# Optimization experiments

Measured on AMD Instinct MI355X. Metric: run time of the kernel, lower is better.

Reference implementation:

```python
import jax, jax.numpy as jnp
import numpy as np

N = 50000      # nodes
E = 800000     # edges (avg degree 16)
D_IN = 128
HID = [128, 64, 32]
C = 2
EPS = 1e-5


def _lin(k, fan_in, fan_out):
    return jax.random.normal(k, (fan_in, fan_out), jnp.float32) / np.float32(np.sqrt(fan_in))


def setup_inputs() -> dict:
    key = jax.random.key(0)
    ks = jax.random.split(key, 40)
    inp = {}
    inp["x"] = jax.random.normal(ks[0], (N, D_IN), jnp.float32)
    inp["edge_index"] = jax.random.randint(ks[1], (2, E), 0, N, dtype=jnp.int32)
    i = 2
    dims = [D_IN] + HID
    for l in range(3):
        di, do = dims[l], dims[l + 1]
        inp[f"W{l}"] = _lin(ks[i], di, do); i += 1
        inp[f"b{l}"] = jnp.zeros((do,), jnp.float32)
        inp[f"bn{l}_g"] = jnp.ones((do,), jnp.float32)
        inp[f"bn{l}_b"] = jnp.zeros((do,), jnp.float32)
        inp[f"bn{l}_m"] = 0.1 * jax.random.normal(ks[i], (do,), jnp.float32); i += 1
        inp[f"bn{l}_v"] = 0.5 + jax.random.uniform(ks[i], (do,), jnp.float32); i += 1
        if di != do:
            inp[f"skip{l}_W"] = _lin(ks[i], di, do); i += 1
            inp[f"skip{l}_b"] = jnp.zeros((do,), jnp.float32)
    inp["cls1_W"] = _lin(ks[i], HID[-1], HID[-1] // 2); i += 1
    inp["cls1_b"] = jnp.zeros((HID[-1] // 2,), jnp.float32)
    inp["cls2_W"] = _lin(ks[i], HID[-1] // 2, C); i += 1
    inp["cls2_b"] = jnp.zeros((C,), jnp.float32)
    return inp


def _gcn_conv(x, W, b, src, dst):
    # PyG GCNConv: add self loops, symmetric deg^{-1/2} normalization.
    h = x @ W                                            # [N, do]
    deg = jax.ops.segment_sum(jnp.ones((E,), h.dtype), dst, num_segments=N) + 1.0  # self loop
    dinv = jax.lax.rsqrt(deg)                            # deg >= 1
    norm = dinv[src] * dinv[dst]                         # [E]
    agg = jax.ops.segment_sum(h[src] * norm[:, None], dst, num_segments=N)
    return agg + h * (dinv * dinv)[:, None] + b          # self-loop msg + bias


def _bn(x, g, b, m, v):
    return (x - m) * jax.lax.rsqrt(v + EPS) * g + b


def reference(x, edge_index,
              W0, b0, bn0_g, bn0_b, bn0_m, bn0_v,
              W1, b1, bn1_g, bn1_b, bn1_m, bn1_v, skip1_W, skip1_b,
              W2, b2, bn2_g, bn2_b, bn2_m, bn2_v, skip2_W, skip2_b,
              cls1_W, cls1_b, cls2_W, cls2_b):
    src, dst = edge_index[0], edge_index[1]
    # layer 0: skip is Identity (128 -> 128)
    res = x
    h = jax.nn.relu(_bn(_gcn_conv(x, W0, b0, src, dst), bn0_g, bn0_b, bn0_m, bn0_v))
    h = h + res
    # layer 1: 128 -> 64, linear skip
    res = h @ skip1_W + skip1_b
    h = jax.nn.relu(_bn(_gcn_conv(h, W1, b1, src, dst), bn1_g, bn1_b, bn1_m, bn1_v))
    h = h + res
    # layer 2: 64 -> 32, linear skip
    res = h @ skip2_W + skip2_b
    h = jax.nn.relu(_bn(_gcn_conv(h, W2, b2, src, dst), bn2_g, bn2_b, bn2_m, bn2_v))
    h = h + res
    # classifier (dropout inactive at inference)
    h = jax.nn.relu(h @ cls1_W + cls1_b)
    logits = h @ cls2_W + cls2_b
    return jax.nn.log_softmax(logits, axis=1)
```

## Files before the change

### kernel.cpp

```cpp
#include <hip/hip_runtime.h>
#include <hip/hip_bf16.h>
#include <math.h>


#define BN_EPS 1e-5f

typedef __attribute__((ext_vector_type(8))) short bf16x8;
typedef __attribute__((ext_vector_type(4))) float f32x4;

static __device__ __forceinline__ float bf2f(unsigned int u16) {
    return __uint_as_float(u16 << 16);
}
static __device__ __forceinline__ unsigned short f2bf(float f) {
    unsigned int b = __float_as_uint(f);
    return (unsigned short)((b + 0x7FFFu + ((b >> 16) & 1u)) >> 16);
}
static __device__ __forceinline__ unsigned int pack2(float a, float b) {
    return (unsigned int)f2bf(a) | ((unsigned int)f2bf(b) << 16);
}
static __device__ __forceinline__ void unpack8(uint4 u, float* f) {
    f[0] = bf2f(u.x & 0xffffu); f[1] = bf2f(u.x >> 16);
    f[2] = bf2f(u.y & 0xffffu); f[3] = bf2f(u.y >> 16);
    f[4] = bf2f(u.z & 0xffffu); f[5] = bf2f(u.z >> 16);
    f[6] = bf2f(u.w & 0xffffu); f[7] = bf2f(u.w >> 16);
}
static __device__ __forceinline__ int swz(int row, int kb, int rowb) {
    return row * rowb + (kb ^ ((row & 7) << 4));
}

__global__ void prep_kernel(int* __restrict__ counts, int N, int nbZero,
                            const float* __restrict__ W0,
                            const float* __restrict__ W1, const float* __restrict__ sk1W,
                            const float* __restrict__ W2, const float* __restrict__ sk2W,
                            unsigned short* __restrict__ Wt0,
                            unsigned short* __restrict__ Wt1,
                            unsigned short* __restrict__ Wt2)
{
    int b = blockIdx.x, tid = threadIdx.x;
    if (b < nbZero) {
        int i = b * 256 + tid;
        if (i < N) counts[i] = 0;
        return;
    }
    b -= nbZero;
    if (b < 64) {
        int idx = b * 256 + tid;
        int m = idx >> 7, k = idx & 127;
        Wt0[idx] = f2bf(W0[(size_t)k * 128 + m]);
        return;
    }
    b -= 64;
    if (b < 64) {
        int idx = b * 256 + tid;
        int m = idx >> 7, k = idx & 127;
        float v = (m < 64) ? W1[(size_t)k * 64 + m] : sk1W[(size_t)k * 64 + (m - 64)];
        Wt1[idx] = f2bf(v);
        return;
    }
    b -= 64;
    {
        int idx = b * 256 + tid;
        int m = idx >> 6, k = idx & 63;
        float v = (m < 32) ? W2[(size_t)k * 32 + m] : sk2W[(size_t)k * 32 + (m - 32)];
        Wt2[idx] = f2bf(v);
    }
}

__global__ void rank_hist_kernel(const int* __restrict__ dst, int* __restrict__ counts,
                                 int* __restrict__ rank, int E) {
    int base = (blockIdx.x * 256 + threadIdx.x) * 4;
    if (base + 3 < E) {
        int4 d = *(const int4*)(dst + base);
        int4 r;
        r.x = atomicAdd(&counts[d.x], 1);
        r.y = atomicAdd(&counts[d.y], 1);
        r.z = atomicAdd(&counts[d.z], 1);
        r.w = atomicAdd(&counts[d.w], 1);
        *(int4*)(rank + base) = r;
    } else {
        for (int e = base; e < E; ++e) rank[e] = atomicAdd(&counts[dst[e]], 1);
    }
}

__global__ void scan_block_kernel(const int* __restrict__ counts, int* __restrict__ excl,
                                  int* __restrict__ bsum, int N) {
    __shared__ int s[256];
    int tid = threadIdx.x;
    int i = blockIdx.x * 256 + tid;
    int v = (i < N) ? counts[i] : 0;
    s[tid] = v;
    __syncthreads();
#pragma unroll
    for (int off = 1; off < 256; off <<= 1) {
        int t = (tid >= off) ? s[tid - off] : 0;
        __syncthreads();
        s[tid] += t;
        __syncthreads();
    }
    if (i < N) excl[i] = s[tid] - v;
    if (tid == 255) bsum[blockIdx.x] = s[255];
}

__global__ void scan_add_kernel(const int* __restrict__ excl, const int* __restrict__ bsum,
                                const int* __restrict__ counts,
                                int* __restrict__ rowptr, float* __restrict__ dinv,
                                int nb, int N, int E) {
    __shared__ int sb[256];
    int tid = threadIdx.x;
    int v = (tid < nb) ? bsum[tid] : 0;
    sb[tid] = v;
    __syncthreads();
#pragma unroll
    for (int off = 1; off < 256; off <<= 1) {
        int t = (tid >= off) ? sb[tid - off] : 0;
        __syncthreads();
        sb[tid] += t;
        __syncthreads();
    }
    int eb = sb[blockIdx.x] - ((blockIdx.x < nb) ? bsum[blockIdx.x] : 0);
    int i = blockIdx.x * 256 + tid;
    if (i < N) {
        rowptr[i] = excl[i] + eb;
        dinv[i]   = rsqrtf((float)counts[i] + 1.0f);
    }
    if (i == N) rowptr[N] = E;
}

__global__ void fill_csr_kernel(const int* __restrict__ src, const int* __restrict__ dst,
                                const int* __restrict__ rank, const int* __restrict__ rowptr,
                                int* __restrict__ csr, int E) {
    int base = (blockIdx.x * 256 + threadIdx.x) * 4;
    if (base + 3 < E) {
        int4 s = *(const int4*)(src + base);
        int4 d = *(const int4*)(dst + base);
        int4 r = *(const int4*)(rank + base);
        csr[rowptr[d.x] + r.x] = s.x;
        csr[rowptr[d.y] + r.y] = s.y;
        csr[rowptr[d.z] + r.z] = s.z;
        csr[rowptr[d.w] + r.w] = s.w;
    } else {
        for (int e = base; e < E; ++e) csr[rowptr[dst[e]] + rank[e]] = src[e];
    }
}

template <int K, int M1, int M2, bool IN_BF16>
__launch_bounds__(256)
__global__ void mfma_gemm_kernel(const float* __restrict__ Xf,
                                 const unsigned short* __restrict__ Xb,
                                 const unsigned short* __restrict__ Wt,
                                 const float* __restrict__ skb,
                                 unsigned short* __restrict__ H,
                                 unsigned short* __restrict__ SK, int N)
{
    constexpr int M    = M1 + M2;
    constexpr int BM   = 8192 / M;
    constexpr int WC   = M / 64;
    constexpr int ROWB = K * 2;
    constexpr int CPR  = K / 8;
    constexpr int WCH  = (M * K) / 2048;

    __shared__ unsigned char XsB[BM * K * 2];
    __shared__ unsigned char WsB[M * K * 2];

    const int tid = threadIdx.x;
    const int r0  = blockIdx.x * BM;

#pragma unroll
    for (int c = 0; c < 4; ++c) {
        int q   = tid + 256 * c;
        int row = q / CPR, kq = q % CPR;
        int grow = r0 + row;
        uint4 u = make_uint4(0u, 0u, 0u, 0u);
        if (IN_BF16) {
            if (grow < N) u = *(const uint4*)(Xb + (size_t)grow * K + kq * 8);
        } else {
            if (grow < N) {
                const float* p = Xf + (size_t)grow * K + kq * 8;
                float4 v0 = *(const float4*)p;
                float4 v1 = *(const float4*)(p + 4);
                u.x = pack2(v0.x, v0.y); u.y = pack2(v0.z, v0.w);
                u.z = pack2(v1.x, v1.y); u.w = pack2(v1.z, v1.w);
            }
        }
        *(uint4*)(XsB + swz(row, kq * 16, ROWB)) = u;
    }
#pragma unroll
    for (int c = 0; c < WCH; ++c) {
        int q = tid + 256 * c;
        int m = q / CPR, kq = q % CPR;
        uint4 u = *(const uint4*)(Wt + (size_t)m * K + kq * 8);
        *(uint4*)(WsB + swz(m, kq * 16, ROWB)) = u;
    }
    __syncthreads();

    const int lane = tid & 63, wid = tid >> 6;
    const int wr = wid / WC, wc = wid % WC;
    const int lrow = lane & 15;
    const int kb   = (lane >> 4) << 4;

    f32x4 acc[2][4];
#pragma unroll
    for (int fi = 0; fi < 2; ++fi)
#pragma unroll
        for (int fj = 0; fj < 4; ++fj)
            acc[fi][fj] = (f32x4){0.f, 0.f, 0.f, 0.f};

#pragma unroll
    for (int ks = 0; ks < K / 32; ++ks) {
        const int kb0 = ks * 64 + kb;
        bf16x8 a0 = *(const bf16x8*)(XsB + swz(wr * 32 +      lrow, kb0, ROWB));
        bf16x8 a1 = *(const bf16x8*)(XsB + swz(wr * 32 + 16 + lrow, kb0, ROWB));
        bf16x8 b0 = *(const bf16x8*)(WsB + swz(wc * 64 +      lrow, kb0, ROWB));
        bf16x8 b1 = *(const bf16x8*)(WsB + swz(wc * 64 + 16 + lrow, kb0, ROWB));
        bf16x8 b2 = *(const bf16x8*)(WsB + swz(wc * 64 + 32 + lrow, kb0, ROWB));
        bf16x8 b3 = *(const bf16x8*)(WsB + swz(wc * 64 + 48 + lrow, kb0, ROWB));
        acc[0][0] = __builtin_amdgcn_mfma_f32_16x16x32_bf16(a0, b0, acc[0][0], 0, 0, 0);
        acc[0][1] = __builtin_amdgcn_mfma_f32_16x16x32_bf16(a0, b1, acc[0][1], 0, 0, 0);
        acc[0][2] = __builtin_amdgcn_mfma_f32_16x16x32_bf16(a0, b2, acc[0][2], 0, 0, 0);
        acc[0][3] = __builtin_amdgcn_mfma_f32_16x16x32_bf16(a0, b3, acc[0][3], 0, 0, 0);
        acc[1][0] = __builtin_amdgcn_mfma_f32_16x16x32_bf16(a1, b0, acc[1][0], 0, 0, 0);
        acc[1][1] = __builtin_amdgcn_mfma_f32_16x16x32_bf16(a1, b1, acc[1][1], 0, 0, 0);
        acc[1][2] = __builtin_amdgcn_mfma_f32_16x16x32_bf16(a1, b2, acc[1][2], 0, 0, 0);
        acc[1][3] = __builtin_amdgcn_mfma_f32_16x16x32_bf16(a1, b3, acc[1][3], 0, 0, 0);
    }

    const int orow0 = r0 + wr * 32 + (lane >> 4) * 4;
#pragma unroll
    for (int fi = 0; fi < 2; ++fi) {
#pragma unroll
        for (int fj = 0; fj < 4; ++fj) {
            const int col = wc * 64 + fj * 16 + lrow;
            const bool conv = (M2 == 0) || (col < M1);
            const float sb = conv ? 0.f : skb[col - M1];
#pragma unroll
            for (int r = 0; r < 4; ++r) {
                const int row = orow0 + fi * 16 + r;
                if (row >= N) continue;
                const float val = acc[fi][fj][r];
                if (conv) H[(size_t)row * M1 + col] = f2bf(val);
                else      SK[(size_t)row * M2 + (col - M1)] = f2bf(val + sb);
            }
        }
    }
}

template <int M, bool OUT_BF16, bool RES_BF16, bool CLS>
__launch_bounds__(256)
__global__ void gather_bn_kernel(const int* __restrict__ rowptr, const int* __restrict__ csr,
                                 const unsigned short* __restrict__ H,
                                 const float* __restrict__ dinv,
                                 const float* __restrict__ bias,
                                 const float* __restrict__ g, const float* __restrict__ b,
                                 const float* __restrict__ m, const float* __restrict__ v,
                                 const void* __restrict__ res, void* __restrict__ out,
                                 const float* __restrict__ cW1, const float* __restrict__ cB1,
                                 const float* __restrict__ cW2, const float* __restrict__ cB2,
                                 int N)
{
    constexpr int TPN = M / 16;
    __shared__ float w1s[512];
    __shared__ float b1s[16];
    __shared__ float w2s[32];
    __shared__ float b2s[2];

    const int tid = threadIdx.x;
    if constexpr (CLS) {
        w1s[tid]       = cW1[tid];
        w1s[tid + 256] = cW1[tid + 256];
        if (tid < 16) b1s[tid] = cB1[tid];
        if (tid < 32) w2s[tid] = cW2[tid];
        if (tid < 2)  b2s[tid] = cB2[tid];
        __syncthreads();
    }

    int gid = blockIdx.x * 256 + tid;
    int n = gid / TPN;
    if (n >= N) return;
    const int c = (gid % TPN) * 16;

    float s[16], o[16];
#pragma unroll
    for (int q = 0; q < 4; ++q) {
        float4 gv = *(const float4*)&g[c + q * 4];
        float4 bv = *(const float4*)&b[c + q * 4];
        float4 mv = *(const float4*)&m[c + q * 4];
        float4 vv = *(const float4*)&v[c + q * 4];
        float4 iv = *(const float4*)&bias[c + q * 4];
        float sv[4] = {gv.x * rsqrtf(vv.x + BN_EPS), gv.y * rsqrtf(vv.y + BN_EPS),
                       gv.z * rsqrtf(vv.z + BN_EPS), gv.w * rsqrtf(vv.w + BN_EPS)};
        float bb[4] = {bv.x, bv.y, bv.z, bv.w};
        float mm[4] = {mv.x, mv.y, mv.z, mv.w};
        float ii[4] = {iv.x, iv.y, iv.z, iv.w};
#pragma unroll
        for (int q2 = 0; q2 < 4; ++q2) {
            s[q * 4 + q2] = sv[q2];
            o[q * 4 + q2] = (ii[q2] - mm[q2]) * sv[q2] + bb[q2];
        }
    }

    const float dn = dinv[n];
    float acc[16];
    {
        uint4 h0 = *(const uint4*)&H[(size_t)n * M + c];
        uint4 h1 = *(const uint4*)&H[(size_t)n * M + c + 8];
        float hf[16];
        unpack8(h0, hf); unpack8(h1, hf + 8);
        const float d2 = dn * dn;
#pragma unroll
        for (int k = 0; k < 16; ++k) acc[k] = hf[k] * d2;
    }

    int p   = rowptr[n];
    int end = rowptr[n + 1];
    for (; p + 3 < end; p += 4) {
        int s0 = csr[p], s1 = csr[p + 1], s2 = csr[p + 2], s3 = csr[p + 3];
        uint4 a0 = *(const uint4*)&H[(size_t)s0 * M + c];
        uint4 a1 = *(const uint4*)&H[(size_t)s0 * M + c + 8];
        uint4 b0_ = *(const uint4*)&H[(size_t)s1 * M + c];
        uint4 b1_ = *(const uint4*)&H[(size_t)s1 * M + c + 8];
        uint4 c0_ = *(const uint4*)&H[(size_t)s2 * M + c];
        uint4 c1_ = *(const uint4*)&H[(size_t)s2 * M + c + 8];
        uint4 d0_ = *(const uint4*)&H[(size_t)s3 * M + c];
        uint4 d1_ = *(const uint4*)&H[(size_t)s3 * M + c + 8];
        float w0 = dinv[s0] * dn, w1 = dinv[s1] * dn;
        float w2 = dinv[s2] * dn, w3 = dinv[s3] * dn;
        float f0[16], f1[16], f2[16], f3[16];
        unpack8(a0, f0); unpack8(a1, f0 + 8);
        unpack8(b0_, f1); unpack8(b1_, f1 + 8);
        unpack8(c0_, f2); unpack8(c1_, f2 + 8);
        unpack8(d0_, f3); unpack8(d1_, f3 + 8);
#pragma unroll
        for (int k = 0; k < 16; ++k) acc[k] = fmaf(f0[k], w0, acc[k]);
#pragma unroll
        for (int k = 0; k < 16; ++k) acc[k] = fmaf(f1[k], w1, acc[k]);
#pragma unroll
        for (int k = 0; k < 16; ++k) acc[k] = fmaf(f2[k], w2, acc[k]);
#pragma unroll
        for (int k = 0; k < 16; ++k) acc[k] = fmaf(f3[k], w3, acc[k]);
    }
    for (; p < end; ++p) {
        int s0 = csr[p];
        uint4 a0 = *(const uint4*)&H[(size_t)s0 * M + c];
        uint4 a1 = *(const uint4*)&H[(size_t)s0 * M + c + 8];
        float w0 = dinv[s0] * dn;
        float f0[16];
        unpack8(a0, f0); unpack8(a1, f0 + 8);
#pragma unroll
        for (int k = 0; k < 16; ++k) acc[k] = fmaf(f0[k], w0, acc[k]);
    }

    float rr[16];
    if constexpr (RES_BF16) {
        const unsigned short* rp = (const unsigned short*)res;
        uint4 r0 = *(const uint4*)&rp[(size_t)n * M + c];
        uint4 r1 = *(const uint4*)&rp[(size_t)n * M + c + 8];
        unpack8(r0, rr); unpack8(r1, rr + 8);
    } else {
        const float* rp = (const float*)res;
#pragma unroll
        for (int q = 0; q < 4; ++q) {
            float4 rv = *(const float4*)&rp[(size_t)n * M + c + q * 4];
            rr[q * 4 + 0] = rv.x; rr[q * 4 + 1] = rv.y;
            rr[q * 4 + 2] = rv.z; rr[q * 4 + 3] = rv.w;
        }
    }

    float outv[16];
#pragma unroll
    for (int k = 0; k < 16; ++k)
        outv[k] = fmaxf(fmaf(acc[k], s[k], o[k]), 0.f) + rr[k];

    if constexpr (CLS) {
        float h[16];
#pragma unroll
        for (int j = 0; j < 16; ++j) h[j] = 0.f;
#pragma unroll
        for (int k = 0; k < 16; ++k)
#pragma unroll
            for (int j = 0; j < 16; ++j)
                h[j] = fmaf(outv[k], w1s[(c + k) * 16 + j], h[j]);
#pragma unroll
        for (int j = 0; j < 16; ++j) h[j] += __shfl_xor(h[j], 1);
        float z0 = b2s[0], z1 = b2s[1];
#pragma unroll
        for (int j = 0; j < 16; ++j) {
            float r = fmaxf(h[j] + b1s[j], 0.f);
            z0 = fmaf(r, w2s[j * 2 + 0], z0);
            z1 = fmaf(r, w2s[j * 2 + 1], z1);
        }
        float mx  = fmaxf(z0, z1);
        float lse = mx + logf(expf(z0 - mx) + expf(z1 - mx));
        if ((tid & 1) == 0) {
            float* op = (float*)out;
            op[(size_t)n * 2 + 0] = z0 - lse;
            op[(size_t)n * 2 + 1] = z1 - lse;
        }
    } else if constexpr (OUT_BF16) {
        unsigned short* op = (unsigned short*)out;
        uint4 u0, u1;
        u0.x = pack2(outv[0], outv[1]);  u0.y = pack2(outv[2], outv[3]);
        u0.z = pack2(outv[4], outv[5]);  u0.w = pack2(outv[6], outv[7]);
        u1.x = pack2(outv[8], outv[9]);  u1.y = pack2(outv[10], outv[11]);
        u1.z = pack2(outv[12], outv[13]); u1.w = pack2(outv[14], outv[15]);
        *(uint4*)&op[(size_t)n * M + c]     = u0;
        *(uint4*)&op[(size_t)n * M + c + 8] = u1;
    } else {
        float* op = (float*)out;
#pragma unroll
        for (int q = 0; q < 4; ++q)
            *(float4*)&op[(size_t)n * M + c + q * 4] =
                make_float4(outv[q * 4], outv[q * 4 + 1], outv[q * 4 + 2], outv[q * 4 + 3]);
    }
}

extern "C" void kernel_launch(void* const* d_in, const int* in_sizes, int n_in,
                              void* d_out, int out_size, void* d_ws, size_t ws_size,
                              hipStream_t stream)
{
    const float* x    = (const float*)d_in[0];
    const int*   edge = (const int*)d_in[1];
    const float* W0   = (const float*)d_in[2];
    const float* b0v  = (const float*)d_in[3];
    const float* bn0g = (const float*)d_in[4];
    const float* bn0b = (const float*)d_in[5];
    const float* bn0m = (const float*)d_in[6];
    const float* bn0v = (const float*)d_in[7];
    const float* W1   = (const float*)d_in[8];
    const float* b1v  = (const float*)d_in[9];
    const float* bn1g = (const float*)d_in[10];
    const float* bn1b = (const float*)d_in[11];
    const float* bn1m = (const float*)d_in[12];
    const float* bn1v = (const float*)d_in[13];
    const float* sk1W = (const float*)d_in[14];
    const float* sk1b = (const float*)d_in[15];
    const float* W2   = (const float*)d_in[16];
    const float* b2v  = (const float*)d_in[17];
    const float* bn2g = (const float*)d_in[18];
    const float* bn2b = (const float*)d_in[19];
    const float* bn2m = (const float*)d_in[20];
    const float* bn2v = (const float*)d_in[21];
    const float* sk2W = (const float*)d_in[22];
    const float* sk2b = (const float*)d_in[23];
    const float* c1W  = (const float*)d_in[24];
    const float* c1b  = (const float*)d_in[25];
    const float* c2W  = (const float*)d_in[26];
    const float* c2b  = (const float*)d_in[27];

    const int N = in_sizes[0] / 128;
    const int E = in_sizes[1] / 2;
    const int* src = edge;
    const int* dst = edge + E;

    char*  ws  = (char*)d_ws;
    size_t off = 0;
    auto alloc = [&](size_t bytes) -> char* {
        char* p = ws + off;
        off += (bytes + 255) & ~(size_t)255;
        return p;
    };
    float*          dinv   = (float*)alloc((size_t)N * 4);
    int*            counts = (int*)  alloc((size_t)N * 4);
    int*            excl   = (int*)  alloc((size_t)N * 4);
    int*            rowptr = (int*)  alloc((size_t)(N + 1) * 4);
    int*            bsum   = (int*)  alloc(256 * 4);
    int*            rank   = (int*)  alloc((size_t)E * 4);
    int*            csr    = (int*)  alloc((size_t)E * 4);
    unsigned short* Hb     = (unsigned short*)alloc((size_t)N * 128 * 2);
    unsigned short* SKb    = (unsigned short*)alloc((size_t)N * 64 * 2);
    unsigned short* Q0     = (unsigned short*)alloc((size_t)N * 128 * 2);
    unsigned short* P1     = (unsigned short*)alloc((size_t)N * 64 * 2);
    unsigned short* Wt0    = (unsigned short*)alloc(128 * 128 * 2);
    unsigned short* Wt1    = (unsigned short*)alloc(128 * 128 * 2);
    unsigned short* Wt2    = (unsigned short*)alloc(64 * 64 * 2);
    (void)ws_size; (void)n_in; (void)out_size;

    dim3 blk(256);
    auto cdiv = [](int a, int b) { return (a + b - 1) / b; };
    const int nbN = cdiv(N, 256);

    prep_kernel<<<nbN + 64 + 64 + 16, blk, 0, stream>>>(
        counts, N, nbN, W0, W1, sk1W, W2, sk2W, Wt0, Wt1, Wt2);

    rank_hist_kernel<<<cdiv(E, 1024), blk, 0, stream>>>(dst, counts, rank, E);
    scan_block_kernel<<<nbN, blk, 0, stream>>>(counts, excl, bsum, N);
    scan_add_kernel<<<cdiv(N + 1, 256), blk, 0, stream>>>(excl, bsum, counts, rowptr, dinv, nbN, N, E);
    fill_csr_kernel<<<cdiv(E, 1024), blk, 0, stream>>>(src, dst, rank, rowptr, csr, E);

    mfma_gemm_kernel<128, 128, 0, false><<<cdiv(N, 64), blk, 0, stream>>>(
        x, nullptr, Wt0, nullptr, Hb, nullptr, N);
    gather_bn_kernel<128, true, false, false><<<cdiv(N * 8, 256), blk, 0, stream>>>(
        rowptr, csr, Hb, dinv, b0v, bn0g, bn0b, bn0m, bn0v, x, Q0,
        nullptr, nullptr, nullptr, nullptr, N);

    mfma_gemm_kernel<128, 64, 64, true><<<cdiv(N, 64), blk, 0, stream>>>(
        nullptr, Q0, Wt1, sk1b, Hb, SKb, N);
    gather_bn_kernel<64, true, true, false><<<cdiv(N * 4, 256), blk, 0, stream>>>(
        rowptr, csr, Hb, dinv, b1v, bn1g, bn1b, bn1m, bn1v, SKb, P1,
        nullptr, nullptr, nullptr, nullptr, N);

    mfma_gemm_kernel<64, 32, 32, true><<<cdiv(N, 128), blk, 0, stream>>>(
        nullptr, P1, Wt2, sk2b, Hb, SKb, N);
    gather_bn_kernel<32, false, true, true><<<cdiv(N * 2, 256), blk, 0, stream>>>(
        rowptr, csr, Hb, dinv, b2v, bn2g, bn2b, bn2m, bn2v, SKb, d_out,
        c1W, c1b, c2W, c2b, N);
}
```

Baseline: 187.9 us.

## Fuse layer-0 GEMM with degree histogram, precompute BN affine, halve gather width

Merges the layer-0 MFMA GEMM and the dst-degree histogram/rank pass into one launch by partitioning blocks, dropping one kernel launch and letting independent work overlap. BatchNorm scale/offset (with conv bias folded in) is precomputed once in the prep kernel instead of being recomputed per thread in each gather. Gather threads now handle 8 channels (one 16-byte load per neighbor) instead of 16, doubling thread count for more memory-level parallelism at the cost of more index/dinv loads per row and an extra shuffle step in the classifier reduction.

```diff
diff --git a/kernel.cpp b/kernel.cpp
--- a/kernel.cpp
+++ b/kernel.cpp
@@ -34,7 +34,17 @@
                             const float* __restrict__ W2, const float* __restrict__ sk2W,
                             unsigned short* __restrict__ Wt0,
                             unsigned short* __restrict__ Wt1,
-                            unsigned short* __restrict__ Wt2)
+                            unsigned short* __restrict__ Wt2,
+                            const float* __restrict__ b0v, const float* __restrict__ bn0g,
+                            const float* __restrict__ bn0b, const float* __restrict__ bn0m,
+                            const float* __restrict__ bn0v,
+                            const float* __restrict__ b1v, const float* __restrict__ bn1g,
+                            const float* __restrict__ bn1b, const float* __restrict__ bn1m,
+                            const float* __restrict__ bn1v,
+                            const float* __restrict__ b2v, const float* __restrict__ bn2g,
+                            const float* __restrict__ bn2b, const float* __restrict__ bn2m,
+                            const float* __restrict__ bn2v,
+                            float* __restrict__ bnS, float* __restrict__ bnO)
 {
     int b = blockIdx.x, tid = threadIdx.x;
     if (b < nbZero) {
@@ -58,27 +68,27 @@
         return;
     }
     b -= 64;
-    {
+    if (b < 16) {
         int idx = b * 256 + tid;
         int m = idx >> 6, k = idx & 63;
         float v = (m < 32) ? W2[(size_t)k * 32 + m] : sk2W[(size_t)k * 32 + (m - 32)];
         Wt2[idx] = f2bf(v);
-    }
-}
-
-__global__ void rank_hist_kernel(const int* __restrict__ dst, int* __restrict__ counts,
-                                 int* __restrict__ rank, int E) {
-    int base = (blockIdx.x * 256 + threadIdx.x) * 4;
-    if (base + 3 < E) {
-        int4 d = *(const int4*)(dst + base);
-        int4 r;
-        r.x = atomicAdd(&counts[d.x], 1);
-        r.y = atomicAdd(&counts[d.y], 1);
-        r.z = atomicAdd(&counts[d.z], 1);
-        r.w = atomicAdd(&counts[d.w], 1);
-        *(int4*)(rank + base) = r;
-    } else {
-        for (int e = base; e < E; ++e) rank[e] = atomicAdd(&counts[dst[e]], 1);
+        return;
+    }
+    if (tid < 128) {
+        float s = bn0g[tid] * rsqrtf(bn0v[tid] + BN_EPS);
+        bnS[tid] = s;
+        bnO[tid] = (b0v[tid] - bn0m[tid]) * s + bn0b[tid];
+    } else if (tid < 192) {
+        int c = tid - 128;
+        float s = bn1g[c] * rsqrtf(bn1v[c] + BN_EPS);
+        bnS[tid] = s;
+        bnO[tid] = (b1v[c] - bn1m[c]) * s + bn1b[c];
+    } else if (tid < 224) {
+        int c = tid - 192;
+        float s = bn2g[c] * rsqrtf(bn2v[c] + BN_EPS);
+        bnS[tid] = s;
+        bnO[tid] = (b2v[c] - bn2m[c]) * s + bn2b[c];
     }
 }
 
@@ -144,13 +154,11 @@
 }
 
 template <int K, int M1, int M2, bool IN_BF16>
-__launch_bounds__(256)
-__global__ void mfma_gemm_kernel(const float* __restrict__ Xf,
-                                 const unsigned short* __restrict__ Xb,
-                                 const unsigned short* __restrict__ Wt,
-                                 const float* __restrict__ skb,
-                                 unsigned short* __restrict__ H,
-                                 unsigned short* __restrict__ SK, int N)
+static __device__ __forceinline__ void gemm_body(
+    const float* __restrict__ Xf, const unsigned short* __restrict__ Xb,
+    const unsigned short* __restrict__ Wt, const float* __restrict__ skb,
+    unsigned short* __restrict__ H, unsigned short* __restrict__ SK, int N,
+    unsigned char* XsB, unsigned char* WsB, int bid)
 {
     constexpr int M    = M1 + M2;
     constexpr int BM   = 8192 / M;
@@ -159,11 +167,8 @@
     constexpr int CPR  = K / 8;
     constexpr int WCH  = (M * K) / 2048;
 
-    __shared__ unsigned char XsB[BM * K * 2];
-    __shared__ unsigned char WsB[M * K * 2];
-
     const int tid = threadIdx.x;
-    const int r0  = blockIdx.x * BM;
+    const int r0  = bid * BM;
 
 #pragma unroll
     for (int c = 0; c < 4; ++c) {
@@ -244,20 +249,62 @@
     }
 }
 
+template <int K, int M1, int M2, bool IN_BF16>
+__launch_bounds__(256)
+__global__ void mfma_gemm_kernel(const float* __restrict__ Xf,
+                                 const unsigned short* __restrict__ Xb,
+                                 const unsigned short* __restrict__ Wt,
+                                 const float* __restrict__ skb,
+                                 unsigned short* __restrict__ H,
+                                 unsigned short* __restrict__ SK, int N)
+{
+    constexpr int M  = M1 + M2;
+    constexpr int BM = 8192 / M;
+    __shared__ unsigned char XsB[BM * K * 2];
+    __shared__ unsigned char WsB[M * K * 2];
+    gemm_body<K, M1, M2, IN_BF16>(Xf, Xb, Wt, skb, H, SK, N, XsB, WsB, blockIdx.x);
+}
+
+__launch_bounds__(256)
+__global__ void gemm0_rank_kernel(const float* __restrict__ X,
+                                  const unsigned short* __restrict__ Wt,
+                                  unsigned short* __restrict__ H, int N, int G0,
+                                  const int* __restrict__ dst, int* __restrict__ counts,
+                                  int* __restrict__ rank, int E)
+{
+    __shared__ unsigned char XsB[64 * 128 * 2];
+    __shared__ unsigned char WsB[128 * 128 * 2];
+    if (blockIdx.x < G0) {
+        gemm_body<128, 128, 0, false>(X, nullptr, Wt, nullptr, H, nullptr, N,
+                                      XsB, WsB, blockIdx.x);
+        return;
+    }
+    int base = ((blockIdx.x - G0) * 256 + threadIdx.x) * 4;
+    if (base + 3 < E) {
+        int4 d = *(const int4*)(dst + base);
+        int4 r;
+        r.x = atomicAdd(&counts[d.x], 1);
+        r.y = atomicAdd(&counts[d.y], 1);
+        r.z = atomicAdd(&counts[d.z], 1);
+        r.w = atomicAdd(&counts[d.w], 1);
+        *(int4*)(rank + base) = r;
+    } else {
+        for (int e = base; e < E; ++e) rank[e] = atomicAdd(&counts[dst[e]], 1);
+    }
+}
+
 template <int M, bool OUT_BF16, bool RES_BF16, bool CLS>
 __launch_bounds__(256)
 __global__ void gather_bn_kernel(const int* __restrict__ rowptr, const int* __restrict__ csr,
                                  const unsigned short* __restrict__ H,
                                  const float* __restrict__ dinv,
-                                 const float* __restrict__ bias,
-                                 const float* __restrict__ g, const float* __restrict__ b,
-                                 const float* __restrict__ m, const float* __restrict__ v,
+                                 const float* __restrict__ bnS, const float* __restrict__ bnO,
                                  const void* __restrict__ res, void* __restrict__ out,
                                  const float* __restrict__ cW1, const float* __restrict__ cB1,
                                  const float* __restrict__ cW2, const float* __restrict__ cB2,
                                  int N)
 {
-    constexpr int TPN = M / 16;
+    constexpr int TPN = M / 8;
     __shared__ float w1s[512];
     __shared__ float b1s[16];
     __shared__ float w2s[32];
@@ -276,98 +323,73 @@
     int gid = blockIdx.x * 256 + tid;
     int n = gid / TPN;
     if (n >= N) return;
-    const int c = (gid % TPN) * 16;
-
-    float s[16], o[16];
-#pragma unroll
-    for (int q = 0; q < 4; ++q) {
-        float4 gv = *(const float4*)&g[c + q * 4];
-        float4 bv = *(const float4*)&b[c + q * 4];
-        float4 mv = *(const float4*)&m[c + q * 4];
-        float4 vv = *(const float4*)&v[c + q * 4];
-        float4 iv = *(const float4*)&bias[c + q * 4];
-        float sv[4] = {gv.x * rsqrtf(vv.x + BN_EPS), gv.y * rsqrtf(vv.y + BN_EPS),
-                       gv.z * rsqrtf(vv.z + BN_EPS), gv.w * rsqrtf(vv.w + BN_EPS)};
-        float bb[4] = {bv.x, bv.y, bv.z, bv.w};
-        float mm[4] = {mv.x, mv.y, mv.z, mv.w};
-        float ii[4] = {iv.x, iv.y, iv.z, iv.w};
-#pragma unroll
-        for (int q2 = 0; q2 < 4; ++q2) {
-            s[q * 4 + q2] = sv[q2];
-            o[q * 4 + q2] = (ii[q2] - mm[q2]) * sv[q2] + bb[q2];
-        }
+    const int c = (gid % TPN) * 8;
+
+    float s[8], o[8];
+    {
+        float4 sa = *(const float4*)&bnS[c], sb_ = *(const float4*)&bnS[c + 4];
+        float4 oa = *(const float4*)&bnO[c], ob_ = *(const float4*)&bnO[c + 4];
+        s[0] = sa.x; s[1] = sa.y; s[2] = sa.z; s[3] = sa.w;
+        s[4] = sb_.x; s[5] = sb_.y; s[6] = sb_.z; s[7] = sb_.w;
+        o[0] = oa.x; o[1] = oa.y; o[2] = oa.z; o[3] = oa.w;
+        o[4] = ob_.x; o[5] = ob_.y; o[6] = ob_.z; o[7] = ob_.w;
     }
 
     const float dn = dinv[n];
-    float acc[16];
-    {
-        uint4 h0 = *(const uint4*)&H[(size_t)n * M + c];
-        uint4 h1 = *(const uint4*)&H[(size_t)n * M + c + 8];
-        float hf[16];
-        unpack8(h0, hf); unpack8(h1, hf + 8);
-        const float d2 = dn * dn;
-#pragma unroll
-        for (int k = 0; k < 16; ++k) acc[k] = hf[k] * d2;
-    }
+    float acc[8], hf[8];
+    uint4 hs = *(const uint4*)&H[(size_t)n * M + c];
+    unpack8(hs, hf);
+    const float d2 = dn * dn;
+#pragma unroll
+    for (int k = 0; k < 8; ++k) acc[k] = hf[k] * d2;
 
     int p   = rowptr[n];
     int end = rowptr[n + 1];
     for (; p + 3 < end; p += 4) {
         int s0 = csr[p], s1 = csr[p + 1], s2 = csr[p + 2], s3 = csr[p + 3];
-        uint4 a0 = *(const uint4*)&H[(size_t)s0 * M + c];
-        uint4 a1 = *(const uint4*)&H[(size_t)s0 * M + c + 8];
-        uint4 b0_ = *(const uint4*)&H[(size_t)s1 * M + c];
-        uint4 b1_ = *(const uint4*)&H[(size_t)s1 * M + c + 8];
-        uint4 c0_ = *(const uint4*)&H[(size_t)s2 * M + c];
-        uint4 c1_ = *(const uint4*)&H[(size_t)s2 * M + c + 8];
-        uint4 d0_ = *(const uint4*)&H[(size_t)s3 * M + c];
-        uint4 d1_ = *(const uint4*)&H[(size_t)s3 * M + c + 8];
+        uint4 h0 = *(const uint4*)&H[(size_t)s0 * M + c];
+        uint4 h1 = *(const uint4*)&H[(size_t)s1 * M + c];
+        uint4 h2 = *(const uint4*)&H[(size_t)s2 * M + c];
+        uint4 h3 = *(const uint4*)&H[(size_t)s3 * M + c];
         float w0 = dinv[s0] * dn, w1 = dinv[s1] * dn;
         float w2 = dinv[s2] * dn, w3 = dinv[s3] * dn;
-        float f0[16], f1[16], f2[16], f3[16];
-        unpack8(a0, f0); unpack8(a1, f0 + 8);
-        unpack8(b0_, f1); unpack8(b1_, f1 + 8);
-        unpack8(c0_, f2); unpack8(c1_, f2 + 8);
-        unpack8(d0_, f3); unpack8(d1_, f3 + 8);
-#pragma unroll
-        for (int k = 0; k < 16; ++k) acc[k] = fmaf(f0[k], w0, acc[k]);
-#pragma unroll
-        for (int k = 0; k < 16; ++k) acc[k] = fmaf(f1[k], w1, acc[k]);
-#pragma unroll
-        for (int k = 0; k < 16; ++k) acc[k] = fmaf(f2[k], w2, acc[k]);
-#pragma unroll
-        for (int k = 0; k < 16; ++k) acc[k] = fmaf(f3[k], w3, acc[k]);
+        float f0[8], f1[8], f2[8], f3[8];
+        unpack8(h0, f0); unpack8(h1, f1); unpack8(h2, f2); unpack8(h3, f3);
+#pragma unroll
+        for (int k = 0; k < 8; ++k) acc[k] = fmaf(f0[k], w0, acc[k]);
+#pragma unroll
+        for (int k = 0; k < 8; ++k) acc[k] = fmaf(f1[k], w1, acc[k]);
+#pragma unroll
+        for (int k = 0; k < 8; ++k) acc[k] = fmaf(f2[k], w2, acc[k]);
+#pragma unroll
+        for (int k = 0; k < 8; ++k) acc[k] = fmaf(f3[k], w3, acc[k]);
     }
     for (; p < end; ++p) {
         int s0 = csr[p];
-        uint4 a0 = *(const uint4*)&H[(size_t)s0 * M + c];
-        uint4 a1 = *(const uint4*)&H[(size_t)s0 * M + c + 8];
+        uint4 h0 = *(const uint4*)&H[(size_t)s0 * M + c];
         float w0 = dinv[s0] * dn;
-        float f0[16];
-        unpack8(a0, f0); unpack8(a1, f0 + 8);
-#pragma unroll
-        for (int k = 0; k < 16; ++k) acc[k] = fmaf(f0[k], w0, acc[k]);
-    }
-
-    float rr[16];
+        float f0[8];
+        unpack8(h0, f0);
+#pragma unroll
+        for (int k = 0; k < 8; ++k) acc[k] = fmaf(f0[k], w0, acc[k]);
+    }
+
+    float rr[8];
     if constexpr (RES_BF16) {
         const unsigned short* rp = (const unsigned short*)res;
         uint4 r0 = *(const uint4*)&rp[(size_t)n * M + c];
-        uint4 r1 = *(const uint4*)&rp[(size_t)n * M + c + 8];
-        unpack8(r0, rr); unpack8(r1, rr + 8);
+        unpack8(r0, rr);
     } else {
         const float* rp = (const float*)res;
-#pragma unroll
-        for (int q = 0; q < 4; ++q) {
-            float4 rv = *(const float4*)&rp[(size_t)n * M + c + q * 4];
-            rr[q * 4 + 0] = rv.x; rr[q * 4 + 1] = rv.y;
-            rr[q * 4 + 2] = rv.z; rr[q * 4 + 3] = rv.w;
-        }
-    }
-
-    float outv[16];
-#pragma unroll
-    for (int k = 0; k < 16; ++k)
+        float4 r0 = *(const float4*)&rp[(size_t)n * M + c];
+        float4 r1 = *(const float4*)&rp[(size_t)n * M + c + 4];
+        rr[0] = r0.x; rr[1] = r0.y; rr[2] = r0.z; rr[3] = r0.w;
+        rr[4] = r1.x; rr[5] = r1.y; rr[6] = r1.z; rr[7] = r1.w;
+    }
+
+    float outv[8];
+#pragma unroll
+    for (int k = 0; k < 8; ++k)
         outv[k] = fmaxf(fmaf(acc[k], s[k], o[k]), 0.f) + rr[k];
 
     if constexpr (CLS) {
@@ -375,12 +397,15 @@
 #pragma unroll
         for (int j = 0; j < 16; ++j) h[j] = 0.f;
 #pragma unroll
-        for (int k = 0; k < 16; ++k)
+        for (int k = 0; k < 8; ++k)
 #pragma unroll
             for (int j = 0; j < 16; ++j)
                 h[j] = fmaf(outv[k], w1s[(c + k) * 16 + j], h[j]);
 #pragma unroll
-        for (int j = 0; j < 16; ++j) h[j] += __shfl_xor(h[j], 1);
+        for (int j = 0; j < 16; ++j) {
+            h[j] += __shfl_xor(h[j], 1);
+            h[j] += __shfl_xor(h[j], 2);
+        }
         float z0 = b2s[0], z1 = b2s[1];
 #pragma unroll
         for (int j = 0; j < 16; ++j) {
@@ -388,28 +413,23 @@
             z0 = fmaf(r, w2s[j * 2 + 0], z0);
             z1 = fmaf(r, w2s[j * 2 + 1], z1);
         }
-        float mx  = fmaxf(z0, z1);
-        float lse = mx + logf(expf(z0 - mx) + expf(z1 - mx));
-        if ((tid & 1) == 0) {
+        if ((tid & 3) == 0) {
+            float mx  = fmaxf(z0, z1);
+            float lse = mx + logf(expf(z0 - mx) + expf(z1 - mx));
             float* op = (float*)out;
             op[(size_t)n * 2 + 0] = z0 - lse;
             op[(size_t)n * 2 + 1] = z1 - lse;
         }
     } else if constexpr (OUT_BF16) {
         unsigned short* op = (unsigned short*)out;
-        uint4 u0, u1;
-        u0.x = pack2(outv[0], outv[1]);  u0.y = pack2(outv[2], outv[3]);
-        u0.z = pack2(outv[4], outv[5]);  u0.w = pack2(outv[6], outv[7]);
-        u1.x = pack2(outv[8], outv[9]);  u1.y = pack2(outv[10], outv[11]);
-        u1.z = pack2(outv[12], outv[13]); u1.w = pack2(outv[14], outv[15]);
-        *(uint4*)&op[(size_t)n * M + c]     = u0;
-        *(uint4*)&op[(size_t)n * M + c + 8] = u1;
+        uint4 u;
+        u.x = pack2(outv[0], outv[1]); u.y = pack2(outv[2], outv[3]);
+        u.z = pack2(outv[4], outv[5]); u.w = pack2(outv[6], outv[7]);
+        *(uint4*)&op[(size_t)n * M + c] = u;
     } else {
         float* op = (float*)out;
-#pragma unroll
-        for (int q = 0; q < 4; ++q)
-            *(float4*)&op[(size_t)n * M + c + q * 4] =
-                make_float4(outv[q * 4], outv[q * 4 + 1], outv[q * 4 + 2], outv[q * 4 + 3]);
+        *(float4*)&op[(size_t)n * M + c]     = make_float4(outv[0], outv[1], outv[2], outv[3]);
+        *(float4*)&op[(size_t)n * M + c + 4] = make_float4(outv[4], outv[5], outv[6], outv[7]);
     }
 }
 
@@ -472,35 +492,39 @@
     unsigned short* Wt0    = (unsigned short*)alloc(128 * 128 * 2);
     unsigned short* Wt1    = (unsigned short*)alloc(128 * 128 * 2);
     unsigned short* Wt2    = (unsigned short*)alloc(64 * 64 * 2);
+    float*          bnS    = (float*)alloc(224 * 4);
+    float*          bnO    = (float*)alloc(224 * 4);
     (void)ws_size; (void)n_in; (void)out_size;
 
     dim3 blk(256);
     auto cdiv = [](int a, int b) { return (a + b - 1) / b; };
     const int nbN = cdiv(N, 256);
 
-    prep_kernel<<<nbN + 64 + 64 + 16, blk, 0, stream>>>(
-        counts, N, nbN, W0, W1, sk1W, W2, sk2W, Wt0, Wt1, Wt2);
-
-    rank_hist_kernel<<<cdiv(E, 1024), blk, 0, stream>>>(dst, counts, rank, E);
+    prep_kernel<<<nbN + 64 + 64 + 16 + 1, blk, 0, stream>>>(
+        counts, N, nbN, W0, W1, sk1W, W2, sk2W, Wt0, Wt1, Wt2,
+        b0v, bn0g, bn0b, bn0m, bn0v,
+        b1v, bn1g, bn1b, bn1m, bn1v,
+        b2v, bn2g, bn2b, bn2m, bn2v, bnS, bnO);
+
+    const int G0 = cdiv(N, 64);
+    const int RB = cdiv(E, 1024);
+    gemm0_rank_kernel<<<G0 + RB, blk, 0, stream>>>(x, Wt0, Hb, N, G0, dst, counts, rank, E);
+
     scan_block_kernel<<<nbN, blk, 0, stream>>>(counts, excl, bsum, N);
     scan_add_kernel<<<cdiv(N + 1, 256), blk, 0, stream>>>(excl, bsum, counts, rowptr, dinv, nbN, N, E);
     fill_csr_kernel<<<cdiv(E, 1024), blk, 0, stream>>>(src, dst, rank, rowptr, csr, E);
 
-    mfma_gemm_kernel<128, 128, 0, false><<<cdiv(N, 64), blk, 0, stream>>>(
-        x, nullptr, Wt0, nullptr, Hb, nullptr, N);
-    gather_bn_kernel<128, true, false, false><<<cdiv(N * 8, 256), blk, 0, stream>>>(
-        rowptr, csr, Hb, dinv, b0v, bn0g, bn0b, bn0m, bn0v, x, Q0,
-        nullptr, nullptr, nullptr, nullptr, N);
+    gather_bn_kernel<128, true, false, false><<<cdiv(N * 16, 256), blk, 0, stream>>>(
+        rowptr, csr, Hb, dinv, bnS, bnO, x, Q0, nullptr, nullptr, nullptr, nullptr, N);
 
     mfma_gemm_kernel<128, 64, 64, true><<<cdiv(N, 64), blk, 0, stream>>>(
         nullptr, Q0, Wt1, sk1b, Hb, SKb, N);
-    gather_bn_kernel<64, true, true, false><<<cdiv(N * 4, 256), blk, 0, stream>>>(
-        rowptr, csr, Hb, dinv, b1v, bn1g, bn1b, bn1m, bn1v, SKb, P1,
+    gather_bn_kernel<64, true, true, false><<<cdiv(N * 8, 256), blk, 0, stream>>>(
+        rowptr, csr, Hb, dinv, bnS + 128, bnO + 128, SKb, P1,
         nullptr, nullptr, nullptr, nullptr, N);
 
     mfma_gemm_kernel<64, 32, 32, true><<<cdiv(N, 128), blk, 0, stream>>>(
         nullptr, P1, Wt2, sk2b, Hb, SKb, N);
-    gather_bn_kernel<32, false, true, true><<<cdiv(N * 2, 256), blk, 0, stream>>>(
-        rowptr, csr, Hb, dinv, b2v, bn2g, bn2b, bn2m, bn2v, SKb, d_out,
-        c1W, c1b, c2W, c2b, N);
-}
+    gather_bn_kernel<32, false, true, true><<<cdiv(N * 4, 256), blk, 0, stream>>>(
+        rowptr, csr, Hb, dinv, bnS + 192, bnO + 192, SKb, d_out, c1W, c1b, c2W, c2b, N);
+}
```

New measurement: 181.6 us. 1.04x faster.
